# Performance work log

Hardware: AMD Instinct MI355X
Metric: run time of the kernel (lower is better)

## Reference

```python
import jax, jax.numpy as jnp
import numpy as np

C = 256
C4 = C // 4  # 64
B = 4
N = 4096
FACTOR = float(np.sqrt(C4))


def setup_inputs() -> dict:
    key = jax.random.key(0)
    k1, k2, k3, k4 = jax.random.split(key, 4)
    x = jax.random.normal(k1, (B, C, N), dtype=jnp.float32)
    # q_conv and k_conv share the SAME weight (tied in the torch module)
    W_qk = jax.random.normal(k2, (C4, C), dtype=jnp.float32) * (1.0 / np.sqrt(C))
    W_v = jax.random.normal(k3, (C4, C), dtype=jnp.float32) * (1.0 / np.sqrt(C))
    b_v = jax.random.normal(k4, (C4,), dtype=jnp.float32) * 0.01
    return {"x": x, "W_qk": W_qk, "W_v": W_v, "b_v": b_v}


def reference(x, W_qk, W_v, b_v):
    # Conv1d with kernel size 1 == per-position linear: [B,C,N] -> [B,C4,N]
    x_q = jnp.einsum('oc,bcn->bon', W_qk, x)          # [B, C4, N]
    x_k = x_q                                          # tied weights: k == q
    x_v = jnp.einsum('oc,bcn->bon', W_v, x) + b_v[None, :, None]  # [B, C4, N]
    # energy = x_k.permute(0,2,1) @ x_q : [B, N, N]
    energy = jnp.einsum('bcn,bcm->bnm', x_k, x_q) / FACTOR
    attention = jax.nn.softmax(energy, axis=-1)        # softmax over last dim
    x_r = jnp.einsum('bcn,bnm->bcm', x_v, attention)   # [B, C4, N]
    return x_r
```

## Files before the change

kernel.cpp:

```cpp
#include <hip/hip_runtime.h>


#define CC 256
#define C4C 64
#define NBATCH 4
#define NN 4096
#define QSCALE 0.42466089f
#define SHIFT2 12.0f

typedef _Float16 f16;
typedef _Float16 half2v __attribute__((ext_vector_type(2)));
typedef _Float16 half4 __attribute__((ext_vector_type(4)));
typedef _Float16 half8 __attribute__((ext_vector_type(8)));
typedef __fp16 fp16x2 __attribute__((ext_vector_type(2)));
typedef float floatx4 __attribute__((ext_vector_type(4)));

static __device__ __forceinline__ half2v pkrtz(float a, float b) {
  fp16x2 r = __builtin_amdgcn_cvt_pkrtz(a, b);
  return __builtin_bit_cast(half2v, r);
}

#define LOADQ(T, A0, A1)                                                   \
  { const f16* p_ = Qb + (size_t)(T) * 1024 + l * 8;                       \
    A0 = *(const half8*)(p_); A1 = *(const half8*)(p_ + 512); }

#define XT_PITCH 264
__global__ __launch_bounds__(256) void qv_kernel(
    const float* __restrict__ x, const float* __restrict__ Wqk,
    const float* __restrict__ Wv, const float* __restrict__ bv,
    f16* __restrict__ Qtb, float* __restrict__ V)
{
  __shared__ __align__(16) f16 xt[32][XT_PITCH];
  const int b = blockIdx.y;
  const int n0 = blockIdx.x * 32;
  const int tid = threadIdx.x;

  {
    const int nq = tid & 7;
    const int cb = tid >> 3;
    const int c = cb * 8;
    const float* xp = x + (size_t)b * CC * NN + n0 + nq * 4;
    float4 r[8];
#pragma unroll
    for (int j = 0; j < 8; ++j)
      r[j] = *(const float4*)(xp + (size_t)(c + j) * NN);
#pragma unroll
    for (int s = 0; s < 4; ++s) {
      half8 h;
#pragma unroll
      for (int j = 0; j < 8; ++j) h[j] = (f16)(((const float*)&r[j])[s]);
      *(half8*)(&xt[nq * 4 + s][c]) = h;
    }
  }

  const int w = tid >> 6, l = tid & 63, lr = l & 15, lg = l >> 4;
  const float* Wsrc = (w < 2) ? Wqk : Wv;
  const int ocb = (w & 1) * 32;
  half8 af[2][8];
#pragma unroll
  for (int t = 0; t < 2; ++t) {
    const float* wp = Wsrc + (size_t)(ocb + t * 16 + lr) * CC + 8 * lg;
#pragma unroll
    for (int kk = 0; kk < 8; ++kk) {
      float4 wa = *(const float4*)(wp + kk * 32);
      float4 wb = *(const float4*)(wp + kk * 32 + 4);
      half8 h;
      h[0] = (f16)wa.x; h[1] = (f16)wa.y; h[2] = (f16)wa.z; h[3] = (f16)wa.w;
      h[4] = (f16)wb.x; h[5] = (f16)wb.y; h[6] = (f16)wb.z; h[7] = (f16)wb.w;
      af[t][kk] = h;
    }
  }

  __syncthreads();

  floatx4 acc[2][2] = {{{0.f,0.f,0.f,0.f},{0.f,0.f,0.f,0.f}},
                       {{0.f,0.f,0.f,0.f},{0.f,0.f,0.f,0.f}}};
#pragma unroll
  for (int nt = 0; nt < 2; ++nt) {
#pragma unroll
    for (int kk = 0; kk < 8; ++kk) {
      half8 bf = *(const half8*)(&xt[nt * 16 + lr][kk * 32 + 8 * lg]);
      acc[0][nt] = __builtin_amdgcn_mfma_f32_16x16x32_f16(af[0][kk], bf, acc[0][nt], 0, 0, 0);
      acc[1][nt] = __builtin_amdgcn_mfma_f32_16x16x32_f16(af[1][kk], bf, acc[1][nt], 0, 0, 0);
    }
  }

  if (w < 2) {
#pragma unroll
    for (int t = 0; t < 2; ++t)
#pragma unroll
      for (int nt = 0; nt < 2; ++nt) {
        int T = (n0 >> 4) + nt;
        int kg = 2 * t + (lg >> 1);
        union { f16 h[4]; unsigned long long u; } q4;
#pragma unroll
        for (int i = 0; i < 4; ++i) q4.h[i] = (f16)(acc[t][nt][i] * QSCALE);
        *(unsigned long long*)(Qtb + (size_t)(b * 256 + T) * 1024 + w * 512
                               + (kg * 16 + lr) * 8 + (lg & 1) * 4) = q4.u;
      }
  } else {
#pragma unroll
    for (int t = 0; t < 2; ++t)
#pragma unroll
      for (int nt = 0; nt < 2; ++nt) {
        int n = n0 + nt * 16 + lr;
        int oc = (w - 2) * 32 + t * 16 + 4 * lg;
#pragma unroll
        for (int i = 0; i < 4; ++i)
          V[((size_t)(b * C4C) + oc + i) * NN + n] = acc[t][nt][i] + bv[oc + i];
      }
  }
}

#define Z_PRELOAD(TBEG)                                                    \
  { _Pragma("unroll")                                                      \
    for (int mt = 0; mt < 8; ++mt) {                                       \
      const f16* p_ = Qb + (size_t)((TBEG) + mt) * 1024 + l * 8;           \
      bb[mt][0] = *(const half8*)(p_);                                     \
      bb[mt][1] = *(const half8*)(p_ + 512);                               \
    } }

#define Z_E(MT, D0, D1)                                                    \
  { D0 = (floatx4){0.f,0.f,0.f,0.f}; D1 = (floatx4){0.f,0.f,0.f,0.f};      \
    D0 = __builtin_amdgcn_mfma_f32_16x16x32_f16(a[0][0], bb[MT][0], D0, 0, 0, 0); \
    D1 = __builtin_amdgcn_mfma_f32_16x16x32_f16(a[1][0], bb[MT][0], D1, 0, 0, 0); \
    D0 = __builtin_amdgcn_mfma_f32_16x16x32_f16(a[0][1], bb[MT][1], D0, 0, 0, 0); \
    D1 = __builtin_amdgcn_mfma_f32_16x16x32_f16(a[1][1], bb[MT][1], D1, 0, 0, 0); }

#define Z_SM(D0, D1)                                                       \
  { _Pragma("unroll")                                                      \
    for (int i = 0; i < 4; ++i) {                                          \
      rs[0][i] += __builtin_amdgcn_exp2f(D0[i]);                           \
      rs[1][i] += __builtin_amdgcn_exp2f(D1[i]); } }

#define Z_TILES17                                                          \
  Z_E(1, dB0, dB1); Z_SM(dA0, dA1);                                        \
  Z_E(2, dA0, dA1); Z_SM(dB0, dB1);                                        \
  Z_E(3, dB0, dB1); Z_SM(dA0, dA1);                                        \
  Z_E(4, dA0, dA1); Z_SM(dB0, dB1);                                        \
  Z_E(5, dB0, dB1); Z_SM(dA0, dA1);                                        \
  Z_E(6, dA0, dA1); Z_SM(dB0, dB1);                                        \
  Z_E(7, dB0, dB1); Z_SM(dA0, dA1);

__global__ __launch_bounds__(256) void z_kernel(
    const f16* __restrict__ Qtb, float* __restrict__ Zp)
{
  __shared__ float zl[4][32];
  const int bx = blockIdx.x;
  const int xcd = bx & 7, slot = bx >> 3;
  const int b = xcd >> 1;
  const int wu = ((xcd & 1) << 7) | slot;
  const int n0 = (wu >> 1) * 32;
  const int mh = wu & 1;
  const int tid = threadIdx.x;
  const int w = tid >> 6, l = tid & 63, lr = l & 15, lg = l >> 4;
  const f16* Qb = Qtb + (size_t)b * 256 * 1024;

  half8 a[2][2];
  LOADQ((n0 >> 4), a[0][0], a[0][1]);
  LOADQ((n0 >> 4) + 1, a[1][0], a[1][1]);

  const int tstr = mh * 128 + w * 32;
  half8 bb[8][2];
  floatx4 dA0, dA1, dB0, dB1;
  float rs[2][4] = {{0.f,0.f,0.f,0.f},{0.f,0.f,0.f,0.f}};

  Z_PRELOAD(tstr);
  Z_E(0, dA0, dA1);
  Z_TILES17;
#pragma unroll 1
  for (int mch = 1; mch < 4; ++mch) {
    Z_PRELOAD(tstr + mch * 8);
    Z_SM(dB0, dB1);
    Z_E(0, dA0, dA1);
    Z_TILES17;
  }
  Z_SM(dB0, dB1);

#pragma unroll
  for (int t = 0; t < 2; ++t)
#pragma unroll
    for (int i = 0; i < 4; ++i) {
      float v = rs[t][i];
      v += __shfl_xor(v, 1); v += __shfl_xor(v, 2);
      v += __shfl_xor(v, 4); v += __shfl_xor(v, 8);
      rs[t][i] = v;
    }
  if (lr == 0) {
#pragma unroll
    for (int t = 0; t < 2; ++t)
#pragma unroll
      for (int i = 0; i < 4; ++i)
        zl[w][16 * t + 4 * lg + i] = rs[t][i];
  }
  __syncthreads();
  if (tid < 32) {
    float s = zl[0][tid] + zl[1][tid] + zl[2][tid] + zl[3][tid];
    Zp[(size_t)mh * NBATCH * NN + b * NN + n0 + tid] = s;
  }
}

__global__ __launch_bounds__(256) void zr_kernel(
    const float* __restrict__ Zp, float* __restrict__ Z)
{
  int i = blockIdx.x * 256 + threadIdx.x;
  Z[i] = Zp[i] + Zp[(size_t)NBATCH * NN + i];
}

__global__ __launch_bounds__(256) void u_kernel(
    const float* __restrict__ V, const float* __restrict__ Z,
    f16* __restrict__ U4)
{
  size_t t = (size_t)blockIdx.x * 256 + threadIdx.x;
  size_t e = t * 8;
  int b = (int)(e >> 18);
  int c = (int)((e >> 12) & 63);
  int n = (int)(e & (NN - 1));
  const float* vp = V + (size_t)b * C4C * NN + (size_t)c * NN + n;
  float4 v0 = *(const float4*)(vp);
  float4 v1 = *(const float4*)(vp + 4);
  const float* zp = Z + b * NN + n;
  float4 z0 = *(const float4*)(zp);
  float4 z1 = *(const float4*)(zp + 4);
  half2v h0 = pkrtz(v0.x * 4096.0f / z0.x, v0.y * 4096.0f / z0.y);
  half2v h1 = pkrtz(v0.z * 4096.0f / z0.z, v0.w * 4096.0f / z0.w);
  half2v h2 = pkrtz(v1.x * 4096.0f / z1.x, v1.y * 4096.0f / z1.y);
  half2v h3 = pkrtz(v1.z * 4096.0f / z1.z, v1.w * 4096.0f / z1.w);
  half8 h = {h0[0], h0[1], h1[0], h1[1], h2[0], h2[1], h3[0], h3[1]};
  *(half8*)(U4 + (size_t)b * (C4C * NN) + (size_t)(n >> 4) * 1024 + c * 16 + (n & 15)) = h;
}

#define LOADU(NB, UA)                                                      \
  { const f16* up_ = Ub + (size_t)(NB) * 1024 + 4 * lg;                    \
    _Pragma("unroll")                                                      \
    for (int cs = 0; cs < 4; ++cs)                                         \
      UA[cs] = *(const half4*)(up_ + (16 * cs + lr) * 16); }

#define E_STEP(A0, A1, DA, DB)                                             \
  { DA = (floatx4){0.f,0.f,0.f,0.f}; DB = (floatx4){0.f,0.f,0.f,0.f};      \
    DA = __builtin_amdgcn_mfma_f32_16x16x32_f16(A0, bq[0][0], DA, 0, 0, 0);\
    DB = __builtin_amdgcn_mfma_f32_16x16x32_f16(A0, bq[1][0], DB, 0, 0, 0);\
    DA = __builtin_amdgcn_mfma_f32_16x16x32_f16(A1, bq[0][1], DA, 0, 0, 0);\
    DB = __builtin_amdgcn_mfma_f32_16x16x32_f16(A1, bq[1][1], DB, 0, 0, 0); }

#define SMPV(DA, DB, UA)                                                   \
  { half2v p0a = pkrtz(__builtin_amdgcn_exp2f(DA[0] - SHIFT2),             \
                       __builtin_amdgcn_exp2f(DA[1] - SHIFT2));            \
    half2v p0b = pkrtz(__builtin_amdgcn_exp2f(DA[2] - SHIFT2),             \
                       __builtin_amdgcn_exp2f(DA[3] - SHIFT2));            \
    half2v p1a = pkrtz(__builtin_amdgcn_exp2f(DB[0] - SHIFT2),             \
                       __builtin_amdgcn_exp2f(DB[1] - SHIFT2));            \
    half2v p1b = pkrtz(__builtin_amdgcn_exp2f(DB[2] - SHIFT2),             \
                       __builtin_amdgcn_exp2f(DB[3] - SHIFT2));            \
    half4 bt0 = {p0a[0], p0a[1], p0b[0], p0b[1]};                          \
    half4 bt1 = {p1a[0], p1a[1], p1b[0], p1b[1]};                          \
    _Pragma("unroll")                                                      \
    for (int cs = 0; cs < 4; ++cs) {                                       \
      o[cs][0] = __builtin_amdgcn_mfma_f32_16x16x16f16(UA[cs], bt0, o[cs][0], 0, 0, 0); \
      o[cs][1] = __builtin_amdgcn_mfma_f32_16x16x16f16(UA[cs], bt1, o[cs][1], 0, 0, 0); } }

__global__ __launch_bounds__(512, 4) void av_kernel(
    const f16* __restrict__ Qtb, const f16* __restrict__ U4,
    float* __restrict__ Out)
{
  __shared__ float red[8][2][16][17];

  const int bx = blockIdx.x;
  const int xcd = bx & 7, slot = bx >> 3;
  const int b = xcd >> 1;
  const int m0 = (((xcd & 1) << 6) | slot) * 32;
  const int tid = threadIdx.x;
  const int w = tid >> 6;
  const int l = tid & 63;
  const int lr = l & 15, lg = l >> 4;

  const f16* Qb = Qtb + (size_t)b * 256 * 1024;
  const f16* Ub = U4 + (size_t)b * (C4C * NN);

  half8 bq[2][2];
  LOADQ((m0 >> 4), bq[0][0], bq[0][1]);
  LOADQ((m0 >> 4) + 1, bq[1][0], bq[1][1]);

  floatx4 o[4][2];
#pragma unroll
  for (int cs = 0; cs < 4; ++cs)
#pragma unroll
    for (int t = 0; t < 2; ++t) o[cs][t] = (floatx4){0.f, 0.f, 0.f, 0.f};

  half8 a0A, a0B, a1A, a1B;
  half4 u0[4], u1[4];
  floatx4 d0A, d0B, d1A, d1B;

  LOADQ(w, a0A, a0B); LOADU(w, u0);
  LOADQ(w + 8, a1A, a1B); LOADU(w + 8, u1);
  E_STEP(a0A, a0B, d0A, d0B);
  int sl = w + 16;
#pragma unroll 1
  for (int k = 0; k < 15; ++k) {
    SMPV(d0A, d0B, u0);
    LOADQ(sl, a0A, a0B); LOADU(sl, u0); sl += 8;
    E_STEP(a1A, a1B, d1A, d1B);
    SMPV(d1A, d1B, u1);
    LOADQ(sl, a1A, a1B); LOADU(sl, u1); sl += 8;
    E_STEP(a0A, a0B, d0A, d0B);
  }
  SMPV(d0A, d0B, u0);
  E_STEP(a1A, a1B, d1A, d1B);
  SMPV(d1A, d1B, u1);

#pragma unroll 1
  for (int cs = 0; cs < 4; ++cs) {
    __syncthreads();
#pragma unroll
    for (int t = 0; t < 2; ++t)
#pragma unroll
      for (int i = 0; i < 4; ++i)
        red[w][t][4 * lg + i][lr] = o[cs][t][i];
    __syncthreads();
    const int t = tid >> 8;
    const int r = (tid >> 4) & 15;
    const int col = tid & 15;
    float ssum = 0.f;
#pragma unroll
    for (int ww = 0; ww < 8; ++ww) ssum += red[ww][t][r][col];
    Out[((size_t)b * C4C + cs * 16 + r) * NN + m0 + t * 16 + col] = ssum;
  }
}

extern "C" void kernel_launch(void* const* d_in, const int* in_sizes, int n_in,
                              void* d_out, int out_size, void* d_ws, size_t ws_size,
                              hipStream_t stream)
{
  const float* x   = (const float*)d_in[0];
  const float* Wqk = (const float*)d_in[1];
  const float* Wv  = (const float*)d_in[2];
  const float* bv  = (const float*)d_in[3];
  float* out = (float*)d_out;

  char* ws = (char*)d_ws;
  f16*   Qtb = (f16*)(ws);
  float* V   = (float*)(ws + (2u << 20));
  float* Z   = (float*)(ws + (6u << 20));
  f16*   U4  = (f16*)(ws + (6u << 20) + (64u << 10));
  float* Zp  = (float*)(ws + (6u << 20) + (64u << 10));

  qv_kernel<<<dim3(128, 4), 256, 0, stream>>>(x, Wqk, Wv, bv, Qtb, V);
  z_kernel<<<dim3(1024), 256, 0, stream>>>(Qtb, Zp);
  zr_kernel<<<dim3(64), 256, 0, stream>>>(Zp, Z);
  u_kernel<<<dim3(512), 256, 0, stream>>>(V, Z, U4);
  av_kernel<<<dim3(512), 512, 0, stream>>>(Qtb, U4, out);
}
```

Baseline: 65.59 us.

## Widen av_kernel tile to 64 columns with 16 waves per block

The attention-times-V kernel now gives each block 64 output columns instead of 32 and runs 16 waves of 1024 threads, on 256 blocks instead of 512. Each loaded Q/U key tile is reused across four column subtiles, which cuts global traffic per unit of work. The software-pipelined double-buffered loop is replaced by a simple per-iteration load-then-compute loop. This adds register pressure (16 accumulators), leaves fewer blocks to fill the GPU, and drops explicit load/compute overlap.

```diff
diff --git a/kernel.cpp b/kernel.cpp
--- a/kernel.cpp
+++ b/kernel.cpp
@@ -236,39 +236,16 @@
     for (int cs = 0; cs < 4; ++cs)                                         \
       UA[cs] = *(const half4*)(up_ + (16 * cs + lr) * 16); }
 
-#define E_STEP(A0, A1, DA, DB)                                             \
-  { DA = (floatx4){0.f,0.f,0.f,0.f}; DB = (floatx4){0.f,0.f,0.f,0.f};      \
-    DA = __builtin_amdgcn_mfma_f32_16x16x32_f16(A0, bq[0][0], DA, 0, 0, 0);\
-    DB = __builtin_amdgcn_mfma_f32_16x16x32_f16(A0, bq[1][0], DB, 0, 0, 0);\
-    DA = __builtin_amdgcn_mfma_f32_16x16x32_f16(A1, bq[0][1], DA, 0, 0, 0);\
-    DB = __builtin_amdgcn_mfma_f32_16x16x32_f16(A1, bq[1][1], DB, 0, 0, 0); }
-
-#define SMPV(DA, DB, UA)                                                   \
-  { half2v p0a = pkrtz(__builtin_amdgcn_exp2f(DA[0] - SHIFT2),             \
-                       __builtin_amdgcn_exp2f(DA[1] - SHIFT2));            \
-    half2v p0b = pkrtz(__builtin_amdgcn_exp2f(DA[2] - SHIFT2),             \
-                       __builtin_amdgcn_exp2f(DA[3] - SHIFT2));            \
-    half2v p1a = pkrtz(__builtin_amdgcn_exp2f(DB[0] - SHIFT2),             \
-                       __builtin_amdgcn_exp2f(DB[1] - SHIFT2));            \
-    half2v p1b = pkrtz(__builtin_amdgcn_exp2f(DB[2] - SHIFT2),             \
-                       __builtin_amdgcn_exp2f(DB[3] - SHIFT2));            \
-    half4 bt0 = {p0a[0], p0a[1], p0b[0], p0b[1]};                          \
-    half4 bt1 = {p1a[0], p1a[1], p1b[0], p1b[1]};                          \
-    _Pragma("unroll")                                                      \
-    for (int cs = 0; cs < 4; ++cs) {                                       \
-      o[cs][0] = __builtin_amdgcn_mfma_f32_16x16x16f16(UA[cs], bt0, o[cs][0], 0, 0, 0); \
-      o[cs][1] = __builtin_amdgcn_mfma_f32_16x16x16f16(UA[cs], bt1, o[cs][1], 0, 0, 0); } }
-
-__global__ __launch_bounds__(512, 4) void av_kernel(
+__global__ __launch_bounds__(1024, 4) void av_kernel(
     const f16* __restrict__ Qtb, const f16* __restrict__ U4,
     float* __restrict__ Out)
 {
-  __shared__ float red[8][2][16][17];
+  __shared__ float red[16][4][16][17];
 
   const int bx = blockIdx.x;
   const int xcd = bx & 7, slot = bx >> 3;
   const int b = xcd >> 1;
-  const int m0 = (((xcd & 1) << 6) | slot) * 32;
+  const int m0 = (((xcd & 1) << 5) | slot) * 64;
   const int tid = threadIdx.x;
   const int w = tid >> 6;
   const int l = tid & 63;
@@ -277,42 +254,46 @@
   const f16* Qb = Qtb + (size_t)b * 256 * 1024;
   const f16* Ub = U4 + (size_t)b * (C4C * NN);
 
-  half8 bq[2][2];
-  LOADQ((m0 >> 4), bq[0][0], bq[0][1]);
-  LOADQ((m0 >> 4) + 1, bq[1][0], bq[1][1]);
-
-  floatx4 o[4][2];
+  half8 bq[4][2];
+#pragma unroll
+  for (int t = 0; t < 4; ++t)
+    LOADQ((m0 >> 4) + t, bq[t][0], bq[t][1]);
+
+  floatx4 o[4][4];
 #pragma unroll
   for (int cs = 0; cs < 4; ++cs)
 #pragma unroll
-    for (int t = 0; t < 2; ++t) o[cs][t] = (floatx4){0.f, 0.f, 0.f, 0.f};
-
-  half8 a0A, a0B, a1A, a1B;
-  half4 u0[4], u1[4];
-  floatx4 d0A, d0B, d1A, d1B;
-
-  LOADQ(w, a0A, a0B); LOADU(w, u0);
-  LOADQ(w + 8, a1A, a1B); LOADU(w + 8, u1);
-  E_STEP(a0A, a0B, d0A, d0B);
-  int sl = w + 16;
+    for (int t = 0; t < 4; ++t) o[cs][t] = (floatx4){0.f, 0.f, 0.f, 0.f};
+
 #pragma unroll 1
-  for (int k = 0; k < 15; ++k) {
-    SMPV(d0A, d0B, u0);
-    LOADQ(sl, a0A, a0B); LOADU(sl, u0); sl += 8;
-    E_STEP(a1A, a1B, d1A, d1B);
-    SMPV(d1A, d1B, u1);
-    LOADQ(sl, a1A, a1B); LOADU(sl, u1); sl += 8;
-    E_STEP(a0A, a0B, d0A, d0B);
-  }
-  SMPV(d0A, d0B, u0);
-  E_STEP(a1A, a1B, d1A, d1B);
-  SMPV(d1A, d1B, u1);
+  for (int it = 0; it < 16; ++it) {
+    const int T = it * 16 + w;
+    half8 a0, a1;
+    LOADQ(T, a0, a1);
+    half4 ua[4];
+    LOADU(T, ua);
+
+#pragma unroll
+    for (int t = 0; t < 4; ++t) {
+      floatx4 d = {0.f, 0.f, 0.f, 0.f};
+      d = __builtin_amdgcn_mfma_f32_16x16x32_f16(a0, bq[t][0], d, 0, 0, 0);
+      d = __builtin_amdgcn_mfma_f32_16x16x32_f16(a1, bq[t][1], d, 0, 0, 0);
+      half2v p01 = pkrtz(__builtin_amdgcn_exp2f(d[0] - SHIFT2),
+                         __builtin_amdgcn_exp2f(d[1] - SHIFT2));
+      half2v p23 = pkrtz(__builtin_amdgcn_exp2f(d[2] - SHIFT2),
+                         __builtin_amdgcn_exp2f(d[3] - SHIFT2));
+      half4 bt = {p01[0], p01[1], p23[0], p23[1]};
+#pragma unroll
+      for (int cs = 0; cs < 4; ++cs)
+        o[cs][t] = __builtin_amdgcn_mfma_f32_16x16x16f16(ua[cs], bt, o[cs][t], 0, 0, 0);
+    }
+  }
 
 #pragma unroll 1
   for (int cs = 0; cs < 4; ++cs) {
     __syncthreads();
 #pragma unroll
-    for (int t = 0; t < 2; ++t)
+    for (int t = 0; t < 4; ++t)
 #pragma unroll
       for (int i = 0; i < 4; ++i)
         red[w][t][4 * lg + i][lr] = o[cs][t][i];
@@ -320,10 +301,10 @@
     const int t = tid >> 8;
     const int r = (tid >> 4) & 15;
     const int col = tid & 15;
-    float ssum = 0.f;
-#pragma unroll
-    for (int ww = 0; ww < 8; ++ww) ssum += red[ww][t][r][col];
-    Out[((size_t)b * C4C + cs * 16 + r) * NN + m0 + t * 16 + col] = ssum;
+    float s = 0.f;
+#pragma unroll
+    for (int ww = 0; ww < 16; ++ww) s += red[ww][t][r][col];
+    Out[((size_t)b * C4C + cs * 16 + r) * NN + m0 + t * 16 + col] = s;
   }
 }
 
@@ -348,5 +329,5 @@
   z_kernel<<<dim3(1024), 256, 0, stream>>>(Qtb, Zp);
   zr_kernel<<<dim3(64), 256, 0, stream>>>(Zp, Z);
   u_kernel<<<dim3(512), 256, 0, stream>>>(V, Z, U4);
-  av_kernel<<<dim3(512), 512, 0, stream>>>(Qtb, U4, out);
-}
+  av_kernel<<<dim3(256), 1024, 0, stream>>>(Qtb, U4, out);
+}
```

Result: slower. 77.34 us (+17.9%).
